# Performance work log

Measured on AMD Instinct MI355X. Metric: run time of the kernel, lower is better.

Reference implementation:

```python
import jax, jax.numpy as jnp
import numpy as np

HIDDEN = 512
SEQ = 2048
BATCH = 64


def setup_inputs() -> dict:
    key = jax.random.key(0)
    k1, k2 = jax.random.split(key)
    x = jax.random.normal(k1, (SEQ, BATCH, HIDDEN), dtype=jnp.float32)
    # weight_hh ~ uniform(0, 1) as in reset_parameters
    weight_hh = jax.random.uniform(k2, (HIDDEN,), dtype=jnp.float32)
    return {"x": x, "weight_hh": weight_hh}


def reference(x, weight_hh):
    # IndRNN (recurrent-only): h_t = relu(x_t + w_hh * h_{t-1})
    # x: [T, B, H], weight_hh: [H]
    h0 = jnp.zeros((x.shape[1], x.shape[2]), dtype=x.dtype)

    def step(h, x_t):
        h_new = jax.nn.relu(x_t + h * weight_hh)  # [B, H]
        return h_new, h_new

    _, outputs = jax.lax.scan(step, h0, x)  # outputs: [T, B, H]
    return outputs
```

## Files before the change

kernel.cpp:

```cpp
#include <hip/hip_runtime.h>


#define HIDDEN 512
#define SEQ 2048
#define BATCH 64

constexpr int NCHAIN = BATCH * HIDDEN;
constexpr int STRIDE = BATCH * HIDDEN;
constexpr int DEPTH = 32;

template <bool PF>
__device__ __forceinline__ void run_chunk(float& hv, const float wh,
                                          const float (&cur)[DEPTH],
                                          float (&nxt)[DEPTH],
                                          const float* __restrict__ xn,
                                          float* __restrict__ o) {
#pragma unroll
  for (int i = 0; i < DEPTH; ++i) {
    if (PF) nxt[i] = __builtin_nontemporal_load(xn + (long)i * STRIDE);
    hv = fmaxf(0.0f, fmaf(wh, hv, cur[i]));
    o[(long)i * STRIDE] = hv;
  }
}

__global__ __launch_bounds__(64) void indrnn_kernel(
    const float* __restrict__ x, const float* __restrict__ w,
    float* __restrict__ out) {
  const int idx = blockIdx.x * 64 + threadIdx.x;
  const float wh = w[idx & (HIDDEN - 1)];
  const float* xp = x + idx;
  float* op = out + idx;

  float bufA[DEPTH], bufB[DEPTH];
#pragma unroll
  for (int i = 0; i < DEPTH; ++i)
    bufA[i] = __builtin_nontemporal_load(xp + (long)i * STRIDE);

  float hv = 0.0f;
  int t = 0;
#pragma unroll 1
  for (; t + 2 * DEPTH < SEQ; t += 2 * DEPTH) {
    run_chunk<true>(hv, wh, bufA, bufB, xp + (long)(t + DEPTH) * STRIDE,
                    op + (long)t * STRIDE);
    run_chunk<true>(hv, wh, bufB, bufA, xp + (long)(t + 2 * DEPTH) * STRIDE,
                    op + (long)(t + DEPTH) * STRIDE);
  }
  run_chunk<true>(hv, wh, bufA, bufB, xp + (long)(t + DEPTH) * STRIDE,
                  op + (long)t * STRIDE);
  run_chunk<false>(hv, wh, bufB, bufA, nullptr,
                   op + (long)(t + DEPTH) * STRIDE);
}

extern "C" void kernel_launch(void* const* d_in, const int* in_sizes, int n_in,
                              void* d_out, int out_size, void* d_ws,
                              size_t ws_size, hipStream_t stream) {
  const float* x = (const float*)d_in[0];
  const float* w = (const float*)d_in[1];
  float* out = (float*)d_out;
  indrnn_kernel<<<NCHAIN / 64, 64, 0, stream>>>(x, w, out);
}
```

Measured before the change: 422.3 us.

## Stage outputs through shared memory for wide nontemporal float2 stores

Blocks grow to 128 chains. Each chunk of 32 timesteps is written into a double-buffered LDS tile, and after a barrier each wave stores half the timesteps as contiguous float2 nontemporal writes. The goal is wider, streaming output stores, which may reduce write traffic overhead on a memory-bound scan. In exchange it adds a __syncthreads per chunk, LDS traffic, and half as many blocks, which may reduce overlap between latency and compute.

Result: faster. 413.8 us (-2.0%).

```diff
diff --git a/kernel.cpp b/kernel.cpp
--- a/kernel.cpp
+++ b/kernel.cpp
@@ -5,50 +5,71 @@
 #define SEQ 2048
 #define BATCH 64
 
+typedef float f2 __attribute__((ext_vector_type(2)));
+
+constexpr int STRIDE = BATCH * HIDDEN;
 constexpr int NCHAIN = BATCH * HIDDEN;
-constexpr int STRIDE = BATCH * HIDDEN;
-constexpr int DEPTH = 32;
+constexpr int CPB = 128;
+constexpr int NBLK = NCHAIN / CPB;
+constexpr int CHUNK = 32;
+constexpr int NCHUNK = SEQ / CHUNK;
+constexpr int S2 = STRIDE / 2;
 
 template <bool PF>
-__device__ __forceinline__ void run_chunk(float& hv, const float wh,
-                                          const float (&cur)[DEPTH],
-                                          float (&nxt)[DEPTH],
-                                          const float* __restrict__ xn,
-                                          float* __restrict__ o) {
+__device__ __forceinline__ void chunk_body(
+    const int k, float& hv, const float wh, const float (&cur)[CHUNK],
+    float (&nxt)[CHUNK], const float* __restrict__ xn,
+    f2* __restrict__ op2, float(*__restrict__ hs)[CHUNK][CPB], const int tid,
+    const int wv, const int lane) {
+  const int par = k & 1;
 #pragma unroll
-  for (int i = 0; i < DEPTH; ++i) {
+  for (int i = 0; i < CHUNK; ++i) {
     if (PF) nxt[i] = __builtin_nontemporal_load(xn + (long)i * STRIDE);
     hv = fmaxf(0.0f, fmaf(wh, hv, cur[i]));
-    o[(long)i * STRIDE] = hv;
+    hs[par][i][tid] = hv;
+  }
+  __syncthreads();
+#pragma unroll
+  for (int j = 0; j < CHUNK / 2; ++j) {
+    const int t = wv * (CHUNK / 2) + j;
+    const f2 v = *(const f2*)&hs[par][t][2 * lane];
+    __builtin_nontemporal_store(v, op2 + (long)(k * CHUNK + t) * S2);
   }
 }
 
-__global__ __launch_bounds__(64) void indrnn_kernel(
+__global__ __launch_bounds__(CPB) void indrnn_wide(
     const float* __restrict__ x, const float* __restrict__ w,
     float* __restrict__ out) {
-  const int idx = blockIdx.x * 64 + threadIdx.x;
-  const float wh = w[idx & (HIDDEN - 1)];
-  const float* xp = x + idx;
-  float* op = out + idx;
+  __shared__ float hs[2][CHUNK][CPB];
 
-  float bufA[DEPTH], bufB[DEPTH];
+  const int tid = threadIdx.x;
+  const int lane = tid & 63;
+  const int wv = tid >> 6;
+  const int chain = blockIdx.x * CPB + tid;
+  const float wh = w[chain & (HIDDEN - 1)];
+  const float* xp = x + chain;
+  f2* op2 = (f2*)out + blockIdx.x * (CPB / 2) + lane;
+
+  float bufA[CHUNK], bufB[CHUNK];
 #pragma unroll
-  for (int i = 0; i < DEPTH; ++i)
+  for (int i = 0; i < CHUNK; ++i)
     bufA[i] = __builtin_nontemporal_load(xp + (long)i * STRIDE);
 
   float hv = 0.0f;
-  int t = 0;
+  int k = 0;
 #pragma unroll 1
-  for (; t + 2 * DEPTH < SEQ; t += 2 * DEPTH) {
-    run_chunk<true>(hv, wh, bufA, bufB, xp + (long)(t + DEPTH) * STRIDE,
-                    op + (long)t * STRIDE);
-    run_chunk<true>(hv, wh, bufB, bufA, xp + (long)(t + 2 * DEPTH) * STRIDE,
-                    op + (long)(t + DEPTH) * STRIDE);
+  for (; k + 2 < NCHUNK; k += 2) {
+    chunk_body<true>(k, hv, wh, bufA, bufB,
+                     xp + (long)(k + 1) * CHUNK * STRIDE, op2, hs, tid, wv,
+                     lane);
+    chunk_body<true>(k + 1, hv, wh, bufB, bufA,
+                     xp + (long)(k + 2) * CHUNK * STRIDE, op2, hs, tid, wv,
+                     lane);
   }
-  run_chunk<true>(hv, wh, bufA, bufB, xp + (long)(t + DEPTH) * STRIDE,
-                  op + (long)t * STRIDE);
-  run_chunk<false>(hv, wh, bufB, bufA, nullptr,
-                   op + (long)(t + DEPTH) * STRIDE);
+  chunk_body<true>(k, hv, wh, bufA, bufB, xp + (long)(k + 1) * CHUNK * STRIDE,
+                   op2, hs, tid, wv, lane);
+  chunk_body<false>(k + 1, hv, wh, bufB, bufA, nullptr, op2, hs, tid, wv,
+                    lane);
 }
 
 extern "C" void kernel_launch(void* const* d_in, const int* in_sizes, int n_in,
@@ -57,5 +78,5 @@
   const float* x = (const float*)d_in[0];
   const float* w = (const float*)d_in[1];
   float* out = (float*)d_out;
-  indrnn_kernel<<<NCHAIN / 64, 64, 0, stream>>>(x, w, out);
+  indrnn_wide<<<NBLK, CPB, 0, stream>>>(x, w, out);
 }
```
